# Optimization experiments

Hardware: AMD Instinct MI355X
Metric: run time of the kernel (lower is better)

Reference implementation:

```python
import jax, jax.numpy as jnp
import numpy as np

N, K, M, DIN, DOUT = 4096, 16, 65536, 256, 256


def setup_inputs() -> dict:
    key = jax.random.key(0)
    ks = jax.random.split(key, 16)
    s = 1.0 / np.sqrt(DOUT)
    x = jax.random.normal(ks[0], (N, DIN), jnp.float32)
    h_tensor = jax.random.normal(ks[1], (M, DOUT), jnp.float32)
    c_tensor = jax.random.normal(ks[2], (M, DOUT), jnp.float32)
    # variable-length child lists: lengths in [1, K], -1 padding like get_nums()
    lengths = jax.random.randint(ks[3], (N,), 1, K + 1)
    idx = jax.random.randint(ks[4], (N, K), 0, M)
    t = jnp.arange(K)[None, :]
    indice = jnp.where(t < lengths[:, None], idx, -1).astype(jnp.int32)
    W_w = jax.random.normal(ks[5], (4 * DOUT, DIN), jnp.float32) * s
    W_b = jax.random.normal(ks[6], (4 * DOUT,), jnp.float32) * s
    h0 = jax.random.normal(ks[7], (4, DOUT), jnp.float32)
    c0 = jax.random.normal(ks[8], (4, DOUT), jnp.float32)
    Wih = jax.random.normal(ks[9], (4, 2, 4 * DOUT, DOUT), jnp.float32) * s
    Whh = jax.random.normal(ks[10], (4, 2, 4 * DOUT, DOUT), jnp.float32) * s
    bih = jax.random.normal(ks[11], (4, 2, 4 * DOUT), jnp.float32) * s
    bhh = jax.random.normal(ks[12], (4, 2, 4 * DOUT), jnp.float32) * s
    fc = jax.random.normal(ks[13], (4, DOUT, 2 * DOUT), jnp.float32) * s
    return dict(x=x, h_tensor=h_tensor, c_tensor=c_tensor, indice=indice,
                W_w=W_w, W_b=W_b, h0=h0, c0=c0, Wih=Wih, Whh=Whh,
                bih=bih, bhh=bhh, fc=fc)


def _lstm_dir(xseq, mask, h_init, c_init, W_ih, W_hh, b, reverse):
    """Masked LSTM over child axis. xseq [N,K,d], mask [N,K] bool. Mimics
    pack_padded_sequence: state frozen and output 0 at padded steps."""
    d = h_init.shape[-1]
    xs = jnp.swapaxes(xseq, 0, 1)   # [K,N,d]
    ms = jnp.swapaxes(mask, 0, 1)   # [K,N]

    def step(carry, inp):
        h, c = carry
        xt, mt = inp
        g = xt @ W_ih.T + h @ W_hh.T + b        # [N,4d], gate order i,f,g,o
        i = jax.nn.sigmoid(g[:, :d])
        f = jax.nn.sigmoid(g[:, d:2 * d])
        u = jnp.tanh(g[:, 2 * d:3 * d])
        o = jax.nn.sigmoid(g[:, 3 * d:])
        c_new = f * c + i * u
        h_new = o * jnp.tanh(c_new)
        m = mt[:, None]
        return (jnp.where(m, h_new, h), jnp.where(m, c_new, c)), jnp.where(m, h_new, 0.0)

    _, ys = jax.lax.scan(step, (h_init, c_init), (xs, ms), reverse=reverse)
    return jnp.swapaxes(ys, 0, 1)   # [N,K,d]


def _bilstm_seq(xseq, mask, h0j, c0j, Wihj, Whhj, bihj, bhhj, fcj):
    n = xseq.shape[0]
    h_init = jnp.broadcast_to(h0j, (n, h0j.shape[-1]))
    c_init = jnp.broadcast_to(c0j, (n, c0j.shape[-1]))
    yf = _lstm_dir(xseq, mask, h_init, c_init, Wihj[0], Whhj[0], bihj[0] + bhhj[0], False)
    yb = _lstm_dir(xseq, mask, h_init, c_init, Wihj[1], Whhj[1], bihj[1] + bhhj[1], True)
    y = jnp.concatenate([yf, yb], axis=-1)      # [N,K,2d]
    return jnp.einsum('nkh,dh->nkd', y, fcj)    # fc (no bias); 0 stays 0 at pads


def reference(x, h_tensor, c_tensor, indice, W_w, W_b, h0, c0, Wih, Whh, bih, bhh, fc):
    mask = indice != -1                           # [N,K]
    length = mask.sum(axis=1)                     # [N], >= 1
    safe_idx = jnp.where(mask, indice, 0)
    h = h_tensor[safe_idx]                        # [N,K,d] gather of child states
    c = c_tensor[safe_idx]
    Wx = x @ W_w.T + W_b                          # [N,4d]
    d = DOUT
    Wf, Wi, Wu, Wo = Wx[:, :d], Wx[:, d:2 * d], Wx[:, 2 * d:3 * d], Wx[:, 3 * d:]
    ys = [_bilstm_seq(h, mask, h0[j], c0[j], Wih[j], Whh[j], bih[j], bhh[j], fc[j])
          for j in range(4)]                      # U_f, U_i, U_u, U_o
    # forget branch: per-child gate, masked sum over children
    branch_f_k = jax.nn.sigmoid(Wf[:, None, :] + ys[0])
    branch_f = jnp.sum(branch_f_k * c * mask[..., None], axis=1)
    # i/u/o use last valid timestep (packed LSTM y_last)
    ar = jnp.arange(x.shape[0])
    last = length - 1
    branch_i = jax.nn.sigmoid(ys[1][ar, last] + Wi)
    branch_u = jnp.tanh(ys[2][ar, last] + Wu)
    branch_o = jax.nn.sigmoid(ys[3][ar, last] + Wo)
    new_c = branch_i * branch_u + branch_f
    new_h = branch_o * jnp.tanh(new_c)
    return new_h, new_c
```

## Files before the change

kernel.cpp:

```cpp
#include <hip/hip_runtime.h>
#include <math.h>

#define N_SEQ 4096
#define KCH   16
#define DM    256
#define G4    1024
#define LP    40
#define EP    68

typedef __attribute__((ext_vector_type(8))) short bf8;
typedef __attribute__((ext_vector_type(4))) float f4;

__device__ __forceinline__ float fast_rcp(float x) { return __builtin_amdgcn_rcpf(x); }
__device__ __forceinline__ float sigf(float x)   { return fast_rcp(1.f + __expf(-x)); }
__device__ __forceinline__ float tanh_f(float x) { return 1.f - 2.f * fast_rcp(1.f + __expf(2.f * x)); }

__device__ __forceinline__ float bf2f(unsigned short u) {
    return __uint_as_float(((unsigned)u) << 16);
}
__device__ __forceinline__ unsigned short f2bf(float f) {
    unsigned u = __float_as_uint(f);
    unsigned r = (u + 0x7fffu + ((u >> 16) & 1u)) >> 16;
    return (unsigned short)r;
}
__device__ __forceinline__ unsigned pack2(float a, float b) {
    return (unsigned)f2bf(a) | ((unsigned)f2bf(b) << 16);
}

#define GLDS(gp, lp) __builtin_amdgcn_global_load_lds( \
    (const __attribute__((address_space(1))) void*)(gp), \
    (__attribute__((address_space(3))) void*)(lp), 16, 0, 0)

template<int NSEG, int LDB>
__device__ __forceinline__ void pass_pipe(
    const unsigned short* const (&segA)[NSEG],
    const unsigned short* const (&segB)[NSEG],
    unsigned short* SM,
    f4 (&acc)[4][4], int wave, int wm, int wn, int jq, int fr)
{
    constexpr int NS = NSEG * 8;

    {
        const unsigned short* A0 = segA[0];
        const unsigned short* B0 = segB[0];
        unsigned short* a = SM + wave * 1024;
        unsigned short* b = SM + 4096 + wave * 1024;
        GLDS(A0, a);            GLDS(A0 + 16 * DM, a + 512);
        GLDS(B0, b);            GLDS(B0 + 16 * LDB, b + 512);
        const unsigned short* A1 = segA[0] + 32;
        const unsigned short* B1 = segB[0] + 32;
        a = SM + 8192 + wave * 1024;
        b = SM + 8192 + 4096 + wave * 1024;
        GLDS(A1, a);            GLDS(A1 + 16 * DM, a + 512);
        GLDS(B1, b);            GLDS(B1 + 16 * LDB, b + 512);
    }
#pragma unroll
    for (int t = 0; t < NS; ++t) {
        if (t < NS - 1)
            asm volatile("s_waitcnt vmcnt(4)" ::: "memory");
        else
            asm volatile("s_waitcnt vmcnt(0)" ::: "memory");
        __builtin_amdgcn_s_barrier();

        if (t + 2 < NS) {
            const int tn = t + 2;
            const unsigned short* A_ = segA[tn >> 3] + (tn & 7) * 32;
            const unsigned short* B_ = segB[tn >> 3] + (tn & 7) * 32;
            unsigned short* a = SM + (tn % 3) * 8192 + wave * 1024;
            unsigned short* b = a + 4096;
            GLDS(A_, a);        GLDS(A_ + 16 * DM, a + 512);
            GLDS(B_, b);        GLDS(B_ + 16 * LDB, b + 512);
        }

        const unsigned short* Ab = SM + (t % 3) * 8192;
        const unsigned short* Bb = Ab + 4096;
        bf8 af[4], bb[4];
#pragma unroll
        for (int i = 0; i < 4; ++i)
            af[i] = *(const bf8*)(Ab + (wm + i * 16 + fr) * 32 + jq);
#pragma unroll
        for (int j = 0; j < 4; ++j)
            bb[j] = *(const bf8*)(Bb + (wn + j * 16 + fr) * 32 + jq);

        __builtin_amdgcn_s_setprio(1);
#pragma unroll
        for (int i = 0; i < 4; ++i)
#pragma unroll
            for (int j = 0; j < 4; ++j)
                acc[i][j] = __builtin_amdgcn_mfma_f32_16x16x32_bf16(
                    af[i], bb[j], acc[i][j], 0, 0, 0);
        __builtin_amdgcn_s_setprio(0);
    }
}

template<int KLEN>
__device__ __forceinline__ void pass_bf(
    const unsigned short* __restrict__ aRow,
    const unsigned short* __restrict__ bRow,
    unsigned short* Asm, unsigned short* Bsm, f4 (&acc)[4][4])
{
    const int tid  = threadIdx.x;
    const int kh   = (tid & 1) * 16;
    const int srow = tid >> 1;
    const int lane = tid & 63, wave = tid >> 6;
    const int wm = (wave >> 1) * 64, wn = (wave & 1) * 64;
    const int fr = lane & 15, fk = (lane >> 4) * 8;
    unsigned short* da = Asm + srow * LP + kh;
    unsigned short* db = Bsm + srow * LP + kh;

    for (int k0 = 0; k0 < KLEN; k0 += 32) {
        __syncthreads();
        *(int4*)(da)     = *(const int4*)(aRow + k0 + kh);
        *(int4*)(da + 8) = *(const int4*)(aRow + k0 + kh + 8);
        *(int4*)(db)     = *(const int4*)(bRow + k0 + kh);
        *(int4*)(db + 8) = *(const int4*)(bRow + k0 + kh + 8);
        __syncthreads();
        bf8 af[4], bb[4];
#pragma unroll
        for (int i = 0; i < 4; ++i)
            af[i] = *(const bf8*)(Asm + (wm + i * 16 + fr) * LP + fk);
#pragma unroll
        for (int j = 0; j < 4; ++j)
            bb[j] = *(const bf8*)(Bsm + (wn + j * 16 + fr) * LP + fk);
#pragma unroll
        for (int i = 0; i < 4; ++i)
#pragma unroll
            for (int j = 0; j < 4; ++j)
                acc[i][j] = __builtin_amdgcn_mfma_f32_16x16x32_bf16(
                    af[i], bb[j], acc[i][j], 0, 0, 0);
    }
}

template<int KLEN>
__device__ __forceinline__ void pass_f32(
    const float* __restrict__ aRow,
    const unsigned short* __restrict__ bRow,
    unsigned short* Asm, unsigned short* Bsm, f4 (&acc)[4][4])
{
    const int tid  = threadIdx.x;
    const int kh   = (tid & 1) * 16;
    const int srow = tid >> 1;
    const int lane = tid & 63, wave = tid >> 6;
    const int wm = (wave >> 1) * 64, wn = (wave & 1) * 64;
    const int fr = lane & 15, fk = (lane >> 4) * 8;
    unsigned short* da = Asm + srow * LP + kh;
    unsigned short* db = Bsm + srow * LP + kh;

    for (int k0 = 0; k0 < KLEN; k0 += 32) {
        __syncthreads();
        {
            const float* s = aRow + k0 + kh;
            float4 v0 = *(const float4*)(s);
            float4 v1 = *(const float4*)(s + 4);
            float4 v2 = *(const float4*)(s + 8);
            float4 v3 = *(const float4*)(s + 12);
            *(int4*)(da)     = make_int4(pack2(v0.x, v0.y), pack2(v0.z, v0.w),
                                         pack2(v1.x, v1.y), pack2(v1.z, v1.w));
            *(int4*)(da + 8) = make_int4(pack2(v2.x, v2.y), pack2(v2.z, v2.w),
                                         pack2(v3.x, v3.y), pack2(v3.z, v3.w));
        }
        *(int4*)(db)     = *(const int4*)(bRow + k0 + kh);
        *(int4*)(db + 8) = *(const int4*)(bRow + k0 + kh + 8);
        __syncthreads();
        bf8 af[4], bb[4];
#pragma unroll
        for (int i = 0; i < 4; ++i)
            af[i] = *(const bf8*)(Asm + (wm + i * 16 + fr) * LP + fk);
#pragma unroll
        for (int j = 0; j < 4; ++j)
            bb[j] = *(const bf8*)(Bsm + (wn + j * 16 + fr) * LP + fk);
#pragma unroll
        for (int i = 0; i < 4; ++i)
#pragma unroll
            for (int j = 0; j < 4; ++j)
                acc[i][j] = __builtin_amdgcn_mfma_f32_16x16x32_bf16(
                    af[i], bb[j], acc[i][j], 0, 0, 0);
    }
}


__global__ __launch_bounds__(256) void k_lastidx(
    const int* __restrict__ indice, int* __restrict__ last_idx)
{
    const int n = blockIdx.x * 256 + threadIdx.x;
    if (n >= N_SEQ) return;
    int len = 0;
#pragma unroll
    for (int k = 0; k < KCH; ++k) len += (indice[n * KCH + k] != -1);
    last_idx[n] = indice[n * KCH + (len - 1)];
}

__global__ __launch_bounds__(1024) void k_hh0_bsum2(
    const float* __restrict__ bih, const float* __restrict__ bhh,
    const float* __restrict__ h0, const float* __restrict__ Whh,
    float* __restrict__ bsum2)
{
    const int jz = blockIdx.x, j = jz + 1;
    const int g = threadIdx.x;
    const int jd = j * 2 + 1;
    const float* wrow = Whh + ((size_t)jd * G4 + g) * DM;
    float s = bih[jd * G4 + g] + bhh[jd * G4 + g];
    for (int h = 0; h < DM; ++h) s = fmaf(h0[j * DM + h], wrow[h], s);
    const int c = (g & 255) * 4 + (g >> 8);
    bsum2[jz * G4 + c] = s;
}

__global__ __launch_bounds__(256) void k_init_states(
    const float* __restrict__ h0, const float* __restrict__ c0,
    unsigned short* __restrict__ hA, float* __restrict__ c_state)
{
    const int row = blockIdx.x;
    const int s = row >> 12;
    const int tree = (s < 4) ? s : 0;
    const int d = threadIdx.x;
    hA[(size_t)row * DM + d]      = f2bf(h0[tree * DM + d]);
    c_state[(size_t)row * DM + d] = c0[tree * DM + d];
}

__global__ __launch_bounds__(256) void k_zero4(float4* __restrict__ p)
{
    p[(size_t)blockIdx.x * 256 + threadIdx.x] = make_float4(0.f, 0.f, 0.f, 0.f);
}

__global__ __launch_bounds__(256) void k_prep_wcat(
    const float* __restrict__ Wih, const float* __restrict__ Whh,
    const float* __restrict__ bih, const float* __restrict__ bhh,
    unsigned short* __restrict__ wcat, float* __restrict__ bsumr)
{
    const int c = blockIdx.x, s = blockIdx.y;
    const int wsel = (s < 4) ? s * 2 : 1;
    const int d = c >> 2, g = c & 3;
    const size_t srcrow = ((size_t)wsel * G4 + g * DM + d) * DM;
    unsigned short* dst = wcat + ((size_t)s * G4 + c) * 512;
    const int t = threadIdx.x;
    dst[t]       = f2bf(Wih[srcrow + t]);
    dst[256 + t] = f2bf(Whh[srcrow + t]);
    if (t == 0)
        bsumr[s * G4 + c] = bih[wsel * G4 + g * DM + d] + bhh[wsel * G4 + g * DM + d];
}

__global__ __launch_bounds__(256) void k_prep_wcat2(
    const float* __restrict__ Wih, unsigned short* __restrict__ wcat2)
{
    const int c = blockIdx.x, jz = blockIdx.y, j = jz + 1;
    const int d = c >> 2, g = c & 3;
    const size_t srcrow = ((size_t)(j * 2 + 1) * G4 + g * DM + d) * DM;
    wcat2[((size_t)jz * G4 + c) * 256 + threadIdx.x] = f2bf(Wih[srcrow + threadIdx.x]);
}

__global__ __launch_bounds__(256) void k_prep_fcb(
    const float* __restrict__ fc, unsigned short* __restrict__ fcb)
{
    const int dout = blockIdx.x, z = blockIdx.y, t = threadIdx.x;
    fcb[((size_t)z * DM + dout) * DM + t] = f2bf(fc[(size_t)dout * 512 + z * DM + t]);
}

__global__ __launch_bounds__(256) void k_prep_fcb2(
    const float* __restrict__ fc, unsigned short* __restrict__ fcb2)
{
    const int dout = blockIdx.x, jz = blockIdx.y, j = jz + 1, t = threadIdx.x;
    const float* src = fc + ((size_t)j * DM + dout) * 512;
    unsigned short* dst = fcb2 + ((size_t)jz * DM + dout) * 512;
    dst[t]       = f2bf(src[t]);
    dst[t + 256] = f2bf(src[t + 256]);
}

__global__ __launch_bounds__(256) void k_prep_wwb(
    const float* __restrict__ W_w, unsigned short* __restrict__ wwb)
{
    const size_t i = (size_t)blockIdx.x * 256 + threadIdx.x;
    wwb[i] = f2bf(W_w[i]);
}

__device__ __forceinline__ void gather_slice(
    const float* __restrict__ h_tensor, const int* __restrict__ indice,
    unsigned short* __restrict__ xbuf, int zz, int kk, int blk)
{
    const int row = blk * 64 + (threadIdx.x >> 2);
    const int cb  = (threadIdx.x & 3) * 64;
    int idx = indice[row * KCH + kk]; if (idx < 0) idx = 0;
    const float* src = h_tensor + (size_t)idx * DM + cb;
    unsigned short* dst = xbuf + ((size_t)zz * N_SEQ + row) * DM + cb;
#pragma unroll
    for (int c = 0; c < 64; c += 4) {
        float4 v = *(const float4*)(src + c);
        *(uint2*)(dst + c) = make_uint2(pack2(v.x, v.y), pack2(v.z, v.w));
    }
}

__global__ __launch_bounds__(256) void k_gather_x0(
    const float* __restrict__ h_tensor, const int* __restrict__ indice,
    unsigned short* __restrict__ xbuf)
{
    const int slice = blockIdx.x >> 6, blk = blockIdx.x & 63;
    gather_slice(h_tensor, indice, xbuf, slice, slice ? (KCH - 1) : 0, blk);
}

__global__ __launch_bounds__(256) void k_scan_merged(
    const unsigned short* __restrict__ xb_cur, unsigned short* __restrict__ xb_nxt,
    const unsigned short* __restrict__ yb_prev, unsigned short* __restrict__ yb_cur,
    const int* __restrict__ indice, const float* __restrict__ h_tensor,
    const unsigned short* __restrict__ h_in, unsigned short* __restrict__ h_out,
    float* __restrict__ c_state,
    const unsigned short* __restrict__ wcat, const float* __restrict__ bsumr,
    const unsigned short* __restrict__ fcb, unsigned short* __restrict__ ys0,
    int r)
{
    __shared__ __align__(16) unsigned short SMEM[24576];

    const int tid  = threadIdx.x;
    const int lane = tid & 63, wave = tid >> 6;
    const int wm = (wave >> 1) * 64, wn = (wave & 1) * 64;
    const int fr = lane & 15;
    const int jq = ((lane >> 4) ^ ((fr >> 1) & 3)) * 8;
    const int lr = wave * 32 + (lane >> 2);
    const int jl = ((lane & 3) ^ ((lane >> 3) & 3)) * 8;

    const int bz = blockIdx.z;

    if (bz == 5) {
        const int id5 = blockIdx.x + 8 * blockIdx.y;
        if (id5 >= 128) {
            const int rr = r + 1;
            if (rr >= KCH) return;
            const int g = id5 - 128;
            const int zz = g >> 6;
            gather_slice(h_tensor, indice, xb_nxt, zz,
                         zz ? (KCH - 1 - rr) : rr, g & 63);
            return;
        }
        if (r == 0) return;
        const int rp = r - 1;
        const int z = id5 >> 6;
        const int kslice = z ? (KCH - 1 - rp) : rp;
        const int row0 = (id5 & 31) * 128;
        const int c0 = ((id5 >> 5) & 1) * 128;

        const unsigned short* ay0 = yb_prev + ((size_t)z * N_SEQ + row0 + lr) * DM + jl;
        const unsigned short* bf0 = fcb + ((size_t)z * DM + c0 + lr) * DM + jl;

        f4 acc[4][4];
#pragma unroll
        for (int i = 0; i < 4; ++i)
#pragma unroll
            for (int j = 0; j < 4; ++j) acc[i][j] = (f4)(0.f);
        {
            const unsigned short* const segA[1] = { ay0 };
            const unsigned short* const segB[1] = { bf0 };
            pass_pipe<1, 256>(segA, segB, SMEM, acc, wave, wm, wn, jq, fr);
        }

#pragma unroll
        for (int i = 0; i < 4; ++i)
#pragma unroll
            for (int j = 0; j < 4; ++j) {
                const int col = c0 + wn + j * 16 + fr;
#pragma unroll
                for (int reg = 0; reg < 4; ++reg) {
                    const int rowg = row0 + wm + i * 16 + (lane >> 4) * 4 + reg;
                    const size_t ix = ((size_t)rowg * KCH + kslice) * DM + col;
                    ys0[ix] = f2bf(bf2f(ys0[ix]) + acc[i][j][reg]);
                }
            }
        return;
    }

    const int s = bz;
    const int k = (s < 4) ? r : (KCH - 1 - r);
    const int z = (s < 4) ? 0 : 1;
    const int bn = blockIdx.y & 7;
    const int bm = (blockIdx.y >> 3) * 8 + blockIdx.x;
    const int row0 = bm * 128, c0 = bn * 128;

    const unsigned short* xz = xb_cur + (size_t)z * N_SEQ * DM;
    const unsigned short* hs_in = h_in + (size_t)s * N_SEQ * DM;
    const unsigned short* ax0 = xz + (size_t)(row0 + lr) * DM + jl;
    const unsigned short* ah0 = hs_in + (size_t)(row0 + lr) * DM + jl;
    const unsigned short* bw0 = wcat + ((size_t)s * G4 + c0 + lr) * 512 + jl;

    f4 acc[4][4];
#pragma unroll
    for (int i = 0; i < 4; ++i)
#pragma unroll
        for (int j = 0; j < 4; ++j) acc[i][j] = (f4)(0.f);

    {
        const unsigned short* const segA[2] = { ax0, ah0 };
        const unsigned short* const segB[2] = { bw0, bw0 + 256 };
        pass_pipe<2, 512>(segA, segB, SMEM, acc, wave, wm, wn, jq, fr);
    }

    float* sc = (float*)SMEM + wave * (16 * EP);
    __syncthreads();
#pragma unroll
    for (int i = 0; i < 4; ++i) {
#pragma unroll
        for (int j = 0; j < 4; ++j) {
            const int colL = j * 16 + fr;
            const int rbase = (lane >> 4) * 4;
#pragma unroll
            for (int reg = 0; reg < 4; ++reg)
                sc[(rbase + reg) * EP + colL] = acc[i][j][reg];
        }
        asm volatile("s_waitcnt lgkmcnt(0)" ::: "memory");
        __builtin_amdgcn_sched_barrier(0);
        const int rowg = row0 + wm + i * 16 + fr;
        const bool m = (indice[rowg * KCH + k] != -1);
#pragma unroll
        for (int q = 0; q < 4; ++q) {
            const int dL = (lane >> 4) + q * 4;
            const f4 gv = *(const f4*)(sc + fr * EP + dL * 4);
            const f4 bb = *(const f4*)(bsumr + s * G4 + c0 + wn + dL * 4);
            const int d = ((c0 + wn) >> 2) + dL;
            const float ii = sigf(gv.x + bb.x);
            const float ff = sigf(gv.y + bb.y);
            const float uu = tanh_f(gv.z + bb.z);
            const float oo = sigf(gv.w + bb.w);
            const size_t cix = ((size_t)s * N_SEQ + rowg) * DM + d;
            const float c_old = c_state[cix];
            const float cn = ff * c_old + ii * uu;
            const float cw = m ? cn : c_old;
            c_state[cix] = cw;
            const float hn = oo * tanh_f(cn);
            const unsigned short hv = m ? f2bf(hn) : hs_in[(size_t)rowg * DM + d];
            h_out[cix] = hv;
            if (s == 0)
                yb_cur[(size_t)rowg * DM + d] = m ? f2bf(hn) : (unsigned short)0;
            else if (s == 4)
                yb_cur[(size_t)(N_SEQ + rowg) * DM + d] = m ? f2bf(hn) : (unsigned short)0;
        }
        asm volatile("s_waitcnt lgkmcnt(0)" ::: "memory");
        __builtin_amdgcn_sched_barrier(0);
    }
}

__global__ __launch_bounds__(256) void k_acc_tail(
    const unsigned short* __restrict__ ybuf, const unsigned short* __restrict__ fcb,
    unsigned short* __restrict__ ys0)
{
    __shared__ __align__(16) unsigned short SMEM[24576];
    const int tid = threadIdx.x;
    const int lane = tid & 63, wave = tid >> 6;
    const int wm = (wave >> 1) * 64, wn = (wave & 1) * 64;
    const int fr = lane & 15;
    const int jq = ((lane >> 4) ^ ((fr >> 1) & 3)) * 8;
    const int lr = wave * 32 + (lane >> 2);
    const int jl = ((lane & 3) ^ ((lane >> 3) & 3)) * 8;

    const int z = blockIdx.z;
    const int kslice = z ? 0 : (KCH - 1);
    const int row0 = blockIdx.y * 128, c0 = blockIdx.x * 128;

    const unsigned short* ay0 = ybuf + ((size_t)z * N_SEQ + row0 + lr) * DM + jl;
    const unsigned short* bf0 = fcb + ((size_t)z * DM + c0 + lr) * DM + jl;

    f4 acc[4][4];
#pragma unroll
    for (int i = 0; i < 4; ++i)
#pragma unroll
        for (int j = 0; j < 4; ++j) acc[i][j] = (f4)(0.f);
    {
        const unsigned short* const segA[1] = { ay0 };
        const unsigned short* const segB[1] = { bf0 };
        pass_pipe<1, 256>(segA, segB, SMEM, acc, wave, wm, wn, jq, fr);
    }

#pragma unroll
    for (int i = 0; i < 4; ++i)
#pragma unroll
        for (int j = 0; j < 4; ++j) {
            const int col = c0 + wn + j * 16 + fr;
#pragma unroll
            for (int reg = 0; reg < 4; ++reg) {
                const int rowg = row0 + wm + i * 16 + (lane >> 4) * 4 + reg;
                const size_t ix = ((size_t)rowg * KCH + kslice) * DM + col;
                ys0[ix] = f2bf(bf2f(ys0[ix]) + acc[i][j][reg]);
            }
        }
}


__global__ __launch_bounds__(256) void k_bwd_mfma(
    const float* __restrict__ h_tensor, const int* __restrict__ last_idx,
    const unsigned short* __restrict__ wcat2, const float* __restrict__ bsum2,
    const float* __restrict__ c0, unsigned short* __restrict__ yb_last)
{
    __shared__ __align__(16) unsigned short SMEM[2 * 128 * LP];
    const int jz = blockIdx.z, j = jz + 1;
    const int row0 = blockIdx.y * 128, c0t = blockIdx.x * 128;
    const int tid = threadIdx.x;
    const int srow = tid >> 1;

    const float* aF = h_tensor + (size_t)last_idx[row0 + srow] * DM;
    const unsigned short* bR = wcat2 + ((size_t)jz * G4 + c0t + srow) * 256;

    f4 acc[4][4];
#pragma unroll
    for (int i = 0; i < 4; ++i)
#pragma unroll
        for (int jj = 0; jj < 4; ++jj) acc[i][jj] = (f4)(0.f);

    pass_f32<256>(aF, bR, SMEM, SMEM + 128 * LP, acc);

    const int lane = tid & 63, wave = tid >> 6;
    const int wm = (wave >> 1) * 64, wn = (wave & 1) * 64;
    float* sc = (float*)SMEM + wave * (16 * EP);

    __syncthreads();
#pragma unroll
    for (int i = 0; i < 4; ++i) {
#pragma unroll
        for (int jj = 0; jj < 4; ++jj) {
            const int colL = jj * 16 + (lane & 15);
            const int rbase = (lane >> 4) * 4;
#pragma unroll
            for (int reg = 0; reg < 4; ++reg)
                sc[(rbase + reg) * EP + colL] = acc[i][jj][reg];
        }
        __syncthreads();
        const int rowg = row0 + wm + i * 16 + (lane & 15);
#pragma unroll
        for (int q = 0; q < 4; ++q) {
            const int dL = (lane >> 4) + q * 4;
            const f4 gv = *(const f4*)(sc + (lane & 15) * EP + dL * 4);
            const f4 bb = *(const f4*)(bsum2 + jz * G4 + c0t + wn + dL * 4);
            const int d = ((c0t + wn) >> 2) + dL;
            const float ii = sigf(gv.x + bb.x);
            const float ff = sigf(gv.y + bb.y);
            const float uu = tanh_f(gv.z + bb.z);
            const float oo = sigf(gv.w + bb.w);
            const float cn = ff * c0[j * DM + d] + ii * uu;
            yb_last[((size_t)jz * N_SEQ + rowg) * DM + d] = f2bf(oo * tanh_f(cn));
        }
        __syncthreads();
    }
}

__global__ __launch_bounds__(256) void k_wx_mfma(
    const float* __restrict__ x, const unsigned short* __restrict__ wwb,
    const float* __restrict__ W_b, unsigned short* __restrict__ Wx)
{
    __shared__ __align__(16) unsigned short SMEM[2 * 128 * LP];
    const int row0 = blockIdx.y * 128, c0 = blockIdx.x * 128;
    const int tid = threadIdx.x;
    const int srow = tid >> 1;

    const float* aF = x + (size_t)(row0 + srow) * DM;
    const unsigned short* bR = wwb + (size_t)(c0 + srow) * DM;

    f4 acc[4][4];
#pragma unroll
    for (int i = 0; i < 4; ++i)
#pragma unroll
        for (int j = 0; j < 4; ++j) acc[i][j] = (f4)(0.f);

    pass_f32<256>(aF, bR, SMEM, SMEM + 128 * LP, acc);

    const int lane = tid & 63, wave = tid >> 6;
    const int wm = (wave >> 1) * 64, wn = (wave & 1) * 64;
#pragma unroll
    for (int i = 0; i < 4; ++i)
#pragma unroll
        for (int j = 0; j < 4; ++j) {
            const int col = c0 + wn + j * 16 + (lane & 15);
            const float bv = W_b[col];
#pragma unroll
            for (int reg = 0; reg < 4; ++reg) {
                const int rowg = row0 + wm + i * 16 + (lane >> 4) * 4 + reg;
                Wx[(size_t)rowg * G4 + col] = f2bf(acc[i][j][reg] + bv);
            }
        }
}

__global__ __launch_bounds__(256) void k_fc_last_mfma(
    const unsigned short* __restrict__ h_final, const unsigned short* __restrict__ yb_last,
    const unsigned short* __restrict__ fcb2, unsigned short* __restrict__ ys_last)
{
    __shared__ __align__(16) unsigned short SMEM[2 * 128 * LP];
    const int jz = blockIdx.z;
    const int row0 = blockIdx.y * 128, c0 = blockIdx.x * 128;
    const int tid = threadIdx.x;
    const int srow = tid >> 1;

    const unsigned short* aH1 = h_final + ((size_t)(1 + jz) * N_SEQ + row0 + srow) * DM;
    const unsigned short* aH2 = yb_last + ((size_t)jz * N_SEQ + row0 + srow) * DM;
    const unsigned short* bR  = fcb2 + ((size_t)jz * DM + c0 + srow) * 512;

    f4 acc[4][4];
#pragma unroll
    for (int i = 0; i < 4; ++i)
#pragma unroll
        for (int j = 0; j < 4; ++j) acc[i][j] = (f4)(0.f);

    pass_bf<256>(aH1, bR, SMEM, SMEM + 128 * LP, acc);
    pass_bf<256>(aH2, bR + 256, SMEM, SMEM + 128 * LP, acc);

    const int lane = tid & 63, wave = tid >> 6;
    const int wm = (wave >> 1) * 64, wn = (wave & 1) * 64;
#pragma unroll
    for (int i = 0; i < 4; ++i)
#pragma unroll
        for (int j = 0; j < 4; ++j) {
            const int col = c0 + wn + j * 16 + (lane & 15);
#pragma unroll
            for (int reg = 0; reg < 4; ++reg) {
                const int rowg = row0 + wm + i * 16 + (lane >> 4) * 4 + reg;
                ys_last[((size_t)jz * N_SEQ + rowg) * DM + col] = f2bf(acc[i][j][reg]);
            }
        }
}

__global__ __launch_bounds__(256) void k_final(
    const unsigned short* __restrict__ Wx, const unsigned short* __restrict__ ys0,
    const unsigned short* __restrict__ ys_last, const float* __restrict__ c_tensor,
    const int* __restrict__ indice, float* __restrict__ out)
{
    const int n = blockIdx.x, d = threadIdx.x;
    const float Wf = bf2f(Wx[(size_t)n * G4 + d]);
    const float Wi = bf2f(Wx[(size_t)n * G4 + DM + d]);
    const float Wu = bf2f(Wx[(size_t)n * G4 + 2 * DM + d]);
    const float Wo = bf2f(Wx[(size_t)n * G4 + 3 * DM + d]);
    float bf = 0.f;
#pragma unroll
    for (int k = 0; k < KCH; ++k) {
        const int id = indice[n * KCH + k];
        if (id >= 0)
            bf += sigf(Wf + bf2f(ys0[((size_t)n * KCH + k) * DM + d])) *
                  c_tensor[(size_t)id * DM + d];
    }
    const float bi = sigf(bf2f(ys_last[((size_t)0 * N_SEQ + n) * DM + d]) + Wi);
    const float bu = tanh_f(bf2f(ys_last[((size_t)1 * N_SEQ + n) * DM + d]) + Wu);
    const float bo = sigf(bf2f(ys_last[((size_t)2 * N_SEQ + n) * DM + d]) + Wo);
    const float nc = bi * bu + bf;
    const float nh = bo * tanh_f(nc);
    out[(size_t)n * DM + d] = nh;
    out[(size_t)N_SEQ * DM + (size_t)n * DM + d] = nc;
}

extern "C" void kernel_launch(void* const* d_in, const int* in_sizes, int n_in,
                              void* d_out, int out_size, void* d_ws, size_t ws_size,
                              hipStream_t stream)
{
    const float* x        = (const float*)d_in[0];
    const float* h_tensor = (const float*)d_in[1];
    const float* c_tensor = (const float*)d_in[2];
    const int*   indice   = (const int*)d_in[3];
    const float* W_w      = (const float*)d_in[4];
    const float* W_b      = (const float*)d_in[5];
    const float* h0       = (const float*)d_in[6];
    const float* c0       = (const float*)d_in[7];
    const float* Wih      = (const float*)d_in[8];
    const float* Whh      = (const float*)d_in[9];
    const float* bih      = (const float*)d_in[10];
    const float* bhh      = (const float*)d_in[11];
    const float* fc       = (const float*)d_in[12];
    float* out = (float*)d_out;

    char* base = (char*)d_ws;
    float*          c_state  = (float*)(base + 0);
    int*            last_idx = (int*)  (base + 20971520);
    float*          bsumr    = (float*)(base + 20987904);
    unsigned short* hA       = (unsigned short*)(base + 21008384);
    unsigned short* hB       = (unsigned short*)(base + 31494144);
    unsigned short* ys0      = (unsigned short*)(base + 41979904);
    unsigned short* ybufA    = (unsigned short*)(base + 75534336);
    unsigned short* ybufB    = (unsigned short*)(base + 79728640);
    unsigned short* xbufA    = (unsigned short*)(base + 83922944);
    unsigned short* fcb      = (unsigned short*)(base + 88117248);
    unsigned short* postbuf  = (unsigned short*)(base + 88379392);
    unsigned short* wcat     = (unsigned short*)(base + 92573696);
    const size_t need = 97816576;
    if (ws_size < need) return;

    unsigned short* xbufB   = postbuf;
    unsigned short* wcat2   = postbuf;
    unsigned short* fcb2    = postbuf + 786432;
    unsigned short* wwb     = postbuf + 1179648;
    float*          bsum2   = (float*)(postbuf + 1441792);
    unsigned short* yb_last = ybufA;
    unsigned short* ys_last = hB;
    unsigned short* WxBuf   = hA;

    k_lastidx<<<16, 256, 0, stream>>>(indice, last_idx);
    k_init_states<<<5 * N_SEQ, 256, 0, stream>>>(h0, c0, hA, c_state);
    k_zero4<<<8192, 256, 0, stream>>>((float4*)ys0);
    k_prep_wcat<<<dim3(G4, 5), 256, 0, stream>>>(Wih, Whh, bih, bhh, wcat, bsumr);
    k_prep_fcb<<<dim3(DM, 2), 256, 0, stream>>>(fc, fcb);
    k_gather_x0<<<128, 256, 0, stream>>>(h_tensor, indice, xbufA);

    for (int r = 0; r < KCH; ++r) {
        const unsigned short* xb_cur = (r & 1) ? xbufB : xbufA;
        unsigned short* xb_nxt       = (r & 1) ? xbufA : xbufB;
        const unsigned short* yb_prev = (r & 1) ? ybufA : ybufB;
        unsigned short* yb_cur        = (r & 1) ? ybufB : ybufA;
        const unsigned short* h_in = (r & 1) ? hB : hA;
        unsigned short* h_out      = (r & 1) ? hA : hB;
        k_scan_merged<<<dim3(8, 32, 6), 256, 0, stream>>>(
            xb_cur, xb_nxt, yb_prev, yb_cur, indice, h_tensor,
            h_in, h_out, c_state, wcat, bsumr, fcb, ys0, r);
    }

    k_acc_tail<<<dim3(2, 32, 2), 256, 0, stream>>>(ybufB, fcb, ys0);

    k_prep_wcat2<<<dim3(G4, 3), 256, 0, stream>>>(Wih, wcat2);
    k_hh0_bsum2<<<3, 1024, 0, stream>>>(bih, bhh, h0, Whh, bsum2);
    k_prep_fcb2<<<dim3(DM, 3), 256, 0, stream>>>(fc, fcb2);
    k_prep_wwb<<<1024, 256, 0, stream>>>(W_w, wwb);

    k_bwd_mfma<<<dim3(8, 32, 3), 256, 0, stream>>>(
        h_tensor, last_idx, wcat2, bsum2, c0, yb_last);
    k_fc_last_mfma<<<dim3(2, 32, 3), 256, 0, stream>>>(hA, yb_last, fcb2, ys_last);
    k_wx_mfma<<<dim3(8, 32), 256, 0, stream>>>(x, wwb, W_b, WxBuf);

    k_final<<<N_SEQ, 256, 0, stream>>>(WxBuf, ys0, ys_last, c_tensor, indice, out);
}
```

Measured before the change: 1.298 ms.

## Deepen GEMM LDS pipeline to five stages and skip masked LSTM state updates

```diff
diff --git a/kernel.cpp b/kernel.cpp
--- a/kernel.cpp
+++ b/kernel.cpp
@@ -31,6 +31,8 @@
     (const __attribute__((address_space(1))) void*)(gp), \
     (__attribute__((address_space(3))) void*)(lp), 16, 0, 0)
 
+#define VW(n) asm volatile("s_waitcnt vmcnt(" #n ")" ::: "memory")
+
 template<int NSEG, int LDB>
 __device__ __forceinline__ void pass_pipe(
     const unsigned short* const (&segA)[NSEG],
@@ -39,40 +41,38 @@
     f4 (&acc)[4][4], int wave, int wm, int wn, int jq, int fr)
 {
     constexpr int NS = NSEG * 8;
-
-    {
-        const unsigned short* A0 = segA[0];
-        const unsigned short* B0 = segB[0];
-        unsigned short* a = SM + wave * 1024;
-        unsigned short* b = SM + 4096 + wave * 1024;
-        GLDS(A0, a);            GLDS(A0 + 16 * DM, a + 512);
-        GLDS(B0, b);            GLDS(B0 + 16 * LDB, b + 512);
-        const unsigned short* A1 = segA[0] + 32;
-        const unsigned short* B1 = segB[0] + 32;
-        a = SM + 8192 + wave * 1024;
-        b = SM + 8192 + 4096 + wave * 1024;
-        GLDS(A1, a);            GLDS(A1 + 16 * DM, a + 512);
-        GLDS(B1, b);            GLDS(B1 + 16 * LDB, b + 512);
+    constexpr int L  = 4;
+    constexpr int NP = (NS < L) ? NS : L;
+
+#pragma unroll
+    for (int p = 0; p < NP; ++p) {
+        const unsigned short* A_ = segA[p >> 3] + (p & 7) * 32;
+        const unsigned short* B_ = segB[p >> 3] + (p & 7) * 32;
+        unsigned short* a = SM + (p % 5) * 8192 + wave * 1024;
+        unsigned short* b = a + 4096;
+        GLDS(A_, a);        GLDS(A_ + 16 * DM, a + 512);
+        GLDS(B_, b);        GLDS(B_ + 16 * LDB, b + 512);
     }
 #pragma unroll
     for (int t = 0; t < NS; ++t) {
-        if (t < NS - 1)
-            asm volatile("s_waitcnt vmcnt(4)" ::: "memory");
-        else
-            asm volatile("s_waitcnt vmcnt(0)" ::: "memory");
+        const int rem = NS - 1 - t;
+        if (rem >= 3)      VW(12);
+        else if (rem == 2) VW(8);
+        else if (rem == 1) VW(4);
+        else               VW(0);
         __builtin_amdgcn_s_barrier();
 
-        if (t + 2 < NS) {
-            const int tn = t + 2;
+        if (t + L < NS) {
+            const int tn = t + L;
             const unsigned short* A_ = segA[tn >> 3] + (tn & 7) * 32;
             const unsigned short* B_ = segB[tn >> 3] + (tn & 7) * 32;
-            unsigned short* a = SM + (tn % 3) * 8192 + wave * 1024;
+            unsigned short* a = SM + (tn % 5) * 8192 + wave * 1024;
             unsigned short* b = a + 4096;
-            GLDS(A_, a);        GLDS(A_ + 16 * DM, a + 512);
-            GLDS(B_, b);        GLDS(B_ + 16 * LDB, b + 512);
-        }
-
-        const unsigned short* Ab = SM + (t % 3) * 8192;
+            GLDS(A_, a);    GLDS(A_ + 16 * DM, a + 512);
+            GLDS(B_, b);    GLDS(B_ + 16 * LDB, b + 512);
+        }
+
+        const unsigned short* Ab = SM + (t % 5) * 8192;
         const unsigned short* Bb = Ab + 4096;
         bf8 af[4], bb[4];
 #pragma unroll
@@ -306,7 +306,7 @@
     const unsigned short* __restrict__ fcb, unsigned short* __restrict__ ys0,
     int r)
 {
-    __shared__ __align__(16) unsigned short SMEM[24576];
+    __shared__ __align__(16) unsigned short SMEM[40960];
 
     const int tid  = threadIdx.x;
     const int lane = tid & 63, wave = tid >> 6;
@@ -392,6 +392,7 @@
 
     float* sc = (float*)SMEM + wave * (16 * EP);
     __syncthreads();
+    const int kprev = (s < 4) ? (k - 1) : (k + 1);
 #pragma unroll
     for (int i = 0; i < 4; ++i) {
 #pragma unroll
@@ -406,28 +407,32 @@
         __builtin_amdgcn_sched_barrier(0);
         const int rowg = row0 + wm + i * 16 + fr;
         const bool m = (indice[rowg * KCH + k] != -1);
+        const bool mpv = (r == 0) ? true : (indice[rowg * KCH + kprev] != -1);
 #pragma unroll
         for (int q = 0; q < 4; ++q) {
             const int dL = (lane >> 4) + q * 4;
             const f4 gv = *(const f4*)(sc + fr * EP + dL * 4);
             const f4 bb = *(const f4*)(bsumr + s * G4 + c0 + wn + dL * 4);
             const int d = ((c0 + wn) >> 2) + dL;
-            const float ii = sigf(gv.x + bb.x);
-            const float ff = sigf(gv.y + bb.y);
-            const float uu = tanh_f(gv.z + bb.z);
-            const float oo = sigf(gv.w + bb.w);
             const size_t cix = ((size_t)s * N_SEQ + rowg) * DM + d;
-            const float c_old = c_state[cix];
-            const float cn = ff * c_old + ii * uu;
-            const float cw = m ? cn : c_old;
-            c_state[cix] = cw;
-            const float hn = oo * tanh_f(cn);
-            const unsigned short hv = m ? f2bf(hn) : hs_in[(size_t)rowg * DM + d];
-            h_out[cix] = hv;
+            unsigned short hv = 0;
+            if (m) {
+                const float ii = sigf(gv.x + bb.x);
+                const float ff = sigf(gv.y + bb.y);
+                const float uu = tanh_f(gv.z + bb.z);
+                const float oo = sigf(gv.w + bb.w);
+                const float c_old = c_state[cix];
+                const float cn = ff * c_old + ii * uu;
+                c_state[cix] = cn;
+                hv = f2bf(oo * tanh_f(cn));
+                h_out[cix] = hv;
+            } else if (mpv) {
+                h_out[cix] = hs_in[(size_t)rowg * DM + d];
+            }
             if (s == 0)
-                yb_cur[(size_t)rowg * DM + d] = m ? f2bf(hn) : (unsigned short)0;
+                yb_cur[(size_t)rowg * DM + d] = m ? hv : (unsigned short)0;
             else if (s == 4)
-                yb_cur[(size_t)(N_SEQ + rowg) * DM + d] = m ? f2bf(hn) : (unsigned short)0;
+                yb_cur[(size_t)(N_SEQ + rowg) * DM + d] = m ? hv : (unsigned short)0;
         }
         asm volatile("s_waitcnt lgkmcnt(0)" ::: "memory");
         __builtin_amdgcn_sched_barrier(0);
@@ -438,7 +443,7 @@
     const unsigned short* __restrict__ ybuf, const unsigned short* __restrict__ fcb,
     unsigned short* __restrict__ ys0)
 {
-    __shared__ __align__(16) unsigned short SMEM[24576];
+    __shared__ __align__(16) unsigned short SMEM[40960];
     const int tid = threadIdx.x;
     const int lane = tid & 63, wave = tid >> 6;
     const int wm = (wave >> 1) * 64, wn = (wave & 1) * 64;
```

Measured after the change: 1.208 ms. 1.07x faster.
